# Performance work log

Measured on AMD Instinct MI355X. Metric: run time of the kernel, lower is better.

Reference implementation:

```python
import jax, jax.numpy as jnp
import numpy as np

B, D = 4096, 128
TAU_PLUS = 0.1
BETA = 1.0
TEMP = 0.5


def _normalize(x):
    return x / jnp.linalg.norm(x, axis=-1, keepdims=True)


def setup_inputs() -> dict:
    key = jax.random.key(0)
    k1, k2, k3, k4 = jax.random.split(key, 4)
    return {
        "img_z1": _normalize(jax.random.normal(k1, (B, D), dtype=jnp.float32)),
        "img_z2": _normalize(jax.random.normal(k2, (B, D), dtype=jnp.float32)),
        "text_z": _normalize(jax.random.normal(k3, (B, D), dtype=jnp.float32)),
        "attr_z": _normalize(jax.random.normal(k4, (B, D), dtype=jnp.float32)),
        "attr_uni": jnp.arange(B, dtype=jnp.int64),
    }


def _hard_negative_inter(o1, o2):
    # HardNegative_Inter with estimator='hard': only cross-modal negatives.
    b = o1.shape[0]
    n = b - 1
    sim = (o1 @ o2.T) / TEMP                       # [B, B]
    mask = ~jnp.eye(b, dtype=bool)                 # drop positive pair (i,i)
    neg = jnp.where(mask, jnp.exp(sim), 0.0)
    # imp = exp(beta * log(neg)) = exp(beta * sim) on masked entries
    imp = jnp.where(mask, jnp.exp(BETA * sim), 0.0)
    pos = jnp.exp(jnp.sum(o1 * o2, axis=-1) / TEMP)
    reweight_neg = jnp.sum(imp * neg, axis=-1) / (jnp.sum(imp, axis=-1) / n)
    ng = (-TAU_PLUS * n * pos + reweight_neg) / (1.0 - TAU_PLUS)
    ng = jnp.maximum(ng, n * np.e ** (-1.0 / TEMP))
    return jnp.mean(-jnp.log(pos / (pos + ng)))


def _hard_negative_intra(o1, o2):
    # HardNegative with estimator='hard': negatives over concat([o1, o2]).
    b = o1.shape[0]
    n = 2 * b - 2
    out = jnp.concatenate([o1, o2], axis=0)        # [2B, D]
    sim = (out @ out.T) / TEMP                     # [2B, 2B]
    idx = jnp.arange(2 * b)
    # mask zeros (i, i) and (i, i +/- B): entries with equal index mod B
    mask = (idx[:, None] % b) != (idx[None, :] % b)
    neg = jnp.where(mask, jnp.exp(sim), 0.0)
    imp = jnp.where(mask, jnp.exp(BETA * sim), 0.0)
    pos = jnp.exp(jnp.sum(o1 * o2, axis=-1) / TEMP)
    pos = jnp.concatenate([pos, pos], axis=0)      # [2B]
    reweight_neg = jnp.sum(imp * neg, axis=-1) / (jnp.sum(imp, axis=-1) / n)
    ng = (-TAU_PLUS * n * pos + reweight_neg) / (1.0 - TAU_PLUS)
    ng = jnp.maximum(ng, n * np.e ** (-1.0 / TEMP))
    return jnp.mean(-jnp.log(pos / (pos + ng)))


def reference(img_z1, img_z2, text_z, attr_z, attr_uni):
    # it/ta disabled (dummyzero); ia (inter) and ii (intra) enabled; numerator = 1
    a = attr_z[attr_uni, :]
    loss_i_a = 0.5 * (
        _hard_negative_inter(img_z1[attr_uni, :], a)
        + _hard_negative_inter(img_z2[attr_uni, :], a)
    )
    loss_inter_modal = loss_i_a / 1.0
    loss_intra_modal = _hard_negative_intra(img_z1, img_z2)
    return loss_inter_modal + loss_intra_modal
```

## Files before the change

### kernel.cpp

```cpp
#include <hip/hip_runtime.h>
#include <hip/hip_bf16.h>

#define BN 4096
#define DD 128

#define SQS 1.69864356f

typedef float f32x4 __attribute__((ext_vector_type(4)));
typedef int   i32x8 __attribute__((ext_vector_type(8)));
typedef int   i32x2 __attribute__((ext_vector_type(2)));

__device__ __forceinline__ float fast_exp2(float x) {
#if __has_builtin(__builtin_amdgcn_exp2f)
    return __builtin_amdgcn_exp2f(x);
#else
    float r;
    asm("v_exp_f32 %0, %1" : "=v"(r) : "v"(x));
    return r;
#endif
}

__global__ __launch_bounds__(256) void prep_kernel(
    const float* __restrict__ z1, const float* __restrict__ z2,
    const float* __restrict__ attr, const int* __restrict__ uni,
    char* __restrict__ Z1f, char* __restrict__ Z2f,
    char* __restrict__ G1f, char* __restrict__ G2f, char* __restrict__ Af,
    float* __restrict__ d1, float* __restrict__ d2, float* __restrict__ d3,
    float* __restrict__ S1, float* __restrict__ S2, float* __restrict__ out)
{
    int p = blockIdx.x;
    int t = threadIdx.x;
    int gid = p * 256 + t;
    if (gid < 4 * BN) { S1[gid] = 0.f; S2[gid] = 0.f; }
    if (gid == 0) out[0] = 0.f;

    int r = t >> 4, q = t & 15;
    int grow = p * 16 + r;
    int arow = uni[grow];

    __shared__ float lp[5][16][128];

    const float* sp[5] = { z1 + (size_t)grow * DD, z2 + (size_t)grow * DD,
                           z1 + (size_t)arow * DD, z2 + (size_t)arow * DD,
                           attr + (size_t)arow * DD };
    float v[5][8];
    #pragma unroll
    for (int m = 0; m < 5; m++) {
        const float4* s4 = (const float4*)(sp[m] + q * 8);
        #pragma unroll
        for (int i = 0; i < 2; i++) {
            float4 f = s4[i];
            v[m][4*i+0] = f.x; v[m][4*i+1] = f.y;
            v[m][4*i+2] = f.z; v[m][4*i+3] = f.w;
        }
    }
    float p1 = 0.f, p2 = 0.f, p3 = 0.f;
    #pragma unroll
    for (int e = 0; e < 8; e++) {
        p3 += v[0][e] * v[1][e];
        p1 += v[2][e] * v[4][e];
        p2 += v[3][e] * v[4][e];
    }
    #pragma unroll
    for (int m = 1; m < 16; m <<= 1) {
        p1 += __shfl_xor(p1, m);
        p2 += __shfl_xor(p2, m);
        p3 += __shfl_xor(p3, m);
    }
    if (q == 0) { d1[grow] = p1; d2[grow] = p2; d3[grow] = p3; }

    #pragma unroll
    for (int m = 0; m < 5; m++)
        #pragma unroll
        for (int e = 0; e < 8; e++)
            lp[m][r][q * 8 + e] = v[m][e] * SQS;
    __syncthreads();

    char* dsts[5] = { Z1f, Z2f, G1f, G2f, Af };
    int rw = (t >> 2) & 15;
    int k0 = 32 * (t >> 6) + (t & 3) * 8;
    #pragma unroll
    for (int m = 0; m < 5; m++) {
        const float* s = &lp[m][rw][k0];
        int w0 = __builtin_amdgcn_cvt_pk_fp8_f32(s[0], s[1], 0, false);
        w0     = __builtin_amdgcn_cvt_pk_fp8_f32(s[2], s[3], w0, true);
        int w1 = __builtin_amdgcn_cvt_pk_fp8_f32(s[4], s[5], 0, false);
        w1     = __builtin_amdgcn_cvt_pk_fp8_f32(s[6], s[7], w1, true);
        i32x2 w = { w0, w1 };
        *reinterpret_cast<i32x2*>(dsts[m] + (size_t)p * 2048 + (size_t)t * 8) = w;
    }
}

__global__ __launch_bounds__(256) void sweep_kernel(
    const char* __restrict__ Z1f, const char* __restrict__ Z2f,
    const char* __restrict__ G1f, const char* __restrict__ G2f,
    const char* __restrict__ Af,
    float* __restrict__ S1, float* __restrict__ S2)
{
    int gwid = blockIdx.x * 4 + (threadIdx.x >> 6);
    int lane = threadIdx.x & 63;

    int job, xblk, ychunk;
    const char *X, *Y;
    if (gwid < 1024) {
        job = gwid >> 9;
        int rem = gwid & 511;
        xblk = rem >> 3;
        ychunk = rem & 7;
        X = job ? G2f : G1f;
        Y = Af;
    } else {
        int g2 = gwid - 1024;
        job = 2 + (g2 >> 10);
        int rem = g2 & 1023;
        xblk = rem >> 4;
        int yc = rem & 15;
        X = (job == 2) ? Z1f : Z2f;
        Y = (yc < 8) ? Z1f : Z2f;
        ychunk = yc & 7;
    }

    size_t laneoff = (size_t)lane * 32;

    const char* xp = X + (size_t)(xblk * 4) * 2048 + laneoff;
    i32x8 xb0 = *reinterpret_cast<const i32x8*>(xp);
    i32x8 xb1 = *reinterpret_cast<const i32x8*>(xp + 2048);
    i32x8 xb2 = *reinterpret_cast<const i32x8*>(xp + 4096);
    i32x8 xb3 = *reinterpret_cast<const i32x8*>(xp + 6144);

    float a0e = 0.f, a0q = 0.f, a1e = 0.f, a1q = 0.f;
    float a2e = 0.f, a2q = 0.f, a3e = 0.f, a3q = 0.f;

    i32x8 yA, yB, yC;
    const char* yb0 = Y + (size_t)ychunk * 65536 + laneoff;

#define LOADY(BUF, PTR) BUF = *reinterpret_cast<const i32x8*>(PTR);

#define COMPY(BUF)                                                           \
    {                                                                        \
        f32x4 c0 = {0.f,0.f,0.f,0.f}, c1 = {0.f,0.f,0.f,0.f};                \
        f32x4 c2 = {0.f,0.f,0.f,0.f}, c3 = {0.f,0.f,0.f,0.f};                \
        c0 = __builtin_amdgcn_mfma_scale_f32_16x16x128_f8f6f4(               \
                 BUF, xb0, c0, 0, 0, 0, 0x7F7F7F7F, 0, 0x7F7F7F7F);          \
        c1 = __builtin_amdgcn_mfma_scale_f32_16x16x128_f8f6f4(               \
                 BUF, xb1, c1, 0, 0, 0, 0x7F7F7F7F, 0, 0x7F7F7F7F);          \
        c2 = __builtin_amdgcn_mfma_scale_f32_16x16x128_f8f6f4(               \
                 BUF, xb2, c2, 0, 0, 0, 0x7F7F7F7F, 0, 0x7F7F7F7F);          \
        c3 = __builtin_amdgcn_mfma_scale_f32_16x16x128_f8f6f4(               \
                 BUF, xb3, c3, 0, 0, 0, 0x7F7F7F7F, 0, 0x7F7F7F7F);          \
        _Pragma("unroll")                                                    \
        for (int q = 0; q < 4; q++) {                                        \
            float e0 = fast_exp2(c0[q]);                                     \
            a0e += e0; a0q = fmaf(e0, e0, a0q);                              \
            float e1 = fast_exp2(c1[q]);                                     \
            a1e += e1; a1q = fmaf(e1, e1, a1q);                              \
            float e2 = fast_exp2(c2[q]);                                     \
            a2e += e2; a2q = fmaf(e2, e2, a2q);                              \
            float e3 = fast_exp2(c3[q]);                                     \
            a3e += e3; a3q = fmaf(e3, e3, a3q);                              \
        }                                                                    \
    }

    LOADY(yA, yb0)
    LOADY(yB, yb0 + 2048)
    #pragma clang loop unroll(disable)
    for (int it = 0; it < 10; it++) {
        const char* pb = yb0 + (size_t)(3 * it) * 2048;
        LOADY(yC, pb + 2 * 2048)
        COMPY(yA)
        LOADY(yA, pb + 3 * 2048)
        COMPY(yB)
        LOADY(yB, pb + 4 * 2048)
        COMPY(yC)
    }
    COMPY(yA)
    COMPY(yB)
#undef LOADY
#undef COMPY

    #pragma unroll
    for (int k = 16; k <= 32; k <<= 1) {
        a0e += __shfl_xor(a0e, k); a0q += __shfl_xor(a0q, k);
        a1e += __shfl_xor(a1e, k); a1q += __shfl_xor(a1q, k);
        a2e += __shfl_xor(a2e, k); a2q += __shfl_xor(a2q, k);
        a3e += __shfl_xor(a3e, k); a3q += __shfl_xor(a3q, k);
    }
    if (lane < 16) {
        int base = job * BN + xblk * 64 + lane;
        atomicAdd(&S1[base],      a0e); atomicAdd(&S2[base],      a0q);
        atomicAdd(&S1[base + 16], a1e); atomicAdd(&S2[base + 16], a1q);
        atomicAdd(&S1[base + 32], a2e); atomicAdd(&S2[base + 32], a2q);
        atomicAdd(&S1[base + 48], a3e); atomicAdd(&S2[base + 48], a3q);
    }
}

__global__ __launch_bounds__(256) void finalize_kernel(
    const float* __restrict__ S1, const float* __restrict__ S2,
    const float* __restrict__ d1, const float* __restrict__ d2,
    const float* __restrict__ d3, float* __restrict__ out)
{
    int idx = blockIdx.x * 256 + threadIdx.x;
    float term = 0.f;
    const float EM2 = 0.13533528323661270f;
    if (idx < 8192) {
        int j = idx >> 12, i = idx & 4095;
        float dv = j ? d2[i] : d1[i];
        float n = 4095.f;
        float pos = __expf(2.f * dv);
        float s1 = S1[j * BN + i] - pos;
        float s2 = S2[j * BN + i] - pos * pos;
        float rw = s2 * n / s1;
        float ng = (-0.1f * n * pos + rw) * (1.f / 0.9f);
        ng = fmaxf(ng, n * EM2);
        term = logf((pos + ng) / pos) * (0.5f / 4096.f);
    } else {
        int i = idx - 8192;
        int ii = i & 4095;
        int job = 2 + (i >> 12);
        float n = 8190.f;
        const float E2 = 7.3890560989306495f, E4 = 54.598150033144236f;
        float pos = __expf(2.f * d3[ii]);
        float s1 = S1[job * BN + ii] - E2 - pos;
        float s2 = S2[job * BN + ii] - E4 - pos * pos;
        float rw = s2 * n / s1;
        float ng = (-0.1f * n * pos + rw) * (1.f / 0.9f);
        ng = fmaxf(ng, n * EM2);
        term = logf((pos + ng) / pos) * (1.f / 8192.f);
    }

    #pragma unroll
    for (int m = 1; m < 64; m <<= 1) term += __shfl_xor(term, m);
    __shared__ float sm[4];
    int wid = threadIdx.x >> 6;
    if ((threadIdx.x & 63) == 0) sm[wid] = term;
    __syncthreads();
    if (threadIdx.x == 0) atomicAdd(out, sm[0] + sm[1] + sm[2] + sm[3]);
}

extern "C" void kernel_launch(void* const* d_in, const int* in_sizes, int n_in,
                              void* d_out, int out_size, void* d_ws, size_t ws_size,
                              hipStream_t stream)
{
    const float* z1   = (const float*)d_in[0];
    const float* z2   = (const float*)d_in[1];
    const float* attr = (const float*)d_in[3];
    const int*   uni  = (const int*)d_in[4];
    float* out = (float*)d_out;

    char* ws = (char*)d_ws;
    size_t matb = (size_t)BN * DD;
    char* Z1f = ws;
    char* Z2f = Z1f + matb;
    char* G1f = Z2f + matb;
    char* G2f = G1f + matb;
    char* Af  = G2f + matb;
    float* S1 = (float*)(ws + 5 * matb);
    float* S2 = S1 + 4 * BN;
    float* d1 = S2 + 4 * BN;
    float* d2 = d1 + BN;
    float* d3 = d2 + BN;

    prep_kernel<<<256, 256, 0, stream>>>(z1, z2, attr, uni,
                                         Z1f, Z2f, G1f, G2f, Af,
                                         d1, d2, d3, S1, S2, out);
    sweep_kernel<<<768, 256, 0, stream>>>(Z1f, Z2f, G1f, G2f, Af, S1, S2);
    finalize_kernel<<<64, 256, 0, stream>>>(S1, S2, d1, d2, d3, out);
}
```

Baseline: 31.30 us.

## Halve per-wave Y chunk, double sweep grid, and pack exp accumulators as float2

Splits each wave's Y range in half (16 tiles instead of 32), doubling the sweep grid to 1536 blocks, so the kernel has more waves to spread across the CUs and better latency hiding. The per-lane accumulators become two-wide float vectors so the adds and FMAs can map to packed FP32 instructions. The cost is twice as many atomicAdds into S1/S2 and per-wave X-tile reloads, plus a shorter loop with less steady-state pipelining.

```diff
diff --git a/kernel.cpp b/kernel.cpp
--- a/kernel.cpp
+++ b/kernel.cpp
@@ -7,6 +7,7 @@
 #define SQS 1.69864356f
 
 typedef float f32x4 __attribute__((ext_vector_type(4)));
+typedef float f32x2 __attribute__((ext_vector_type(2)));
 typedef int   i32x8 __attribute__((ext_vector_type(8)));
 typedef int   i32x2 __attribute__((ext_vector_type(2)));
 
@@ -102,22 +103,22 @@
 
     int job, xblk, ychunk;
     const char *X, *Y;
-    if (gwid < 1024) {
-        job = gwid >> 9;
-        int rem = gwid & 511;
-        xblk = rem >> 3;
-        ychunk = rem & 7;
+    if (gwid < 2048) {
+        job = gwid >> 10;
+        int rem = gwid & 1023;
+        xblk = rem >> 4;
+        ychunk = rem & 15;
         X = job ? G2f : G1f;
         Y = Af;
     } else {
-        int g2 = gwid - 1024;
-        job = 2 + (g2 >> 10);
-        int rem = g2 & 1023;
-        xblk = rem >> 4;
-        int yc = rem & 15;
+        int g2 = gwid - 2048;
+        job = 2 + (g2 >> 11);
+        int rem = g2 & 2047;
+        xblk = rem >> 5;
+        int yc = rem & 31;
         X = (job == 2) ? Z1f : Z2f;
-        Y = (yc < 8) ? Z1f : Z2f;
-        ychunk = yc & 7;
+        Y = (yc < 16) ? Z1f : Z2f;
+        ychunk = yc & 15;
     }
 
     size_t laneoff = (size_t)lane * 32;
@@ -128,11 +129,11 @@
     i32x8 xb2 = *reinterpret_cast<const i32x8*>(xp + 4096);
     i32x8 xb3 = *reinterpret_cast<const i32x8*>(xp + 6144);
 
-    float a0e = 0.f, a0q = 0.f, a1e = 0.f, a1q = 0.f;
-    float a2e = 0.f, a2q = 0.f, a3e = 0.f, a3q = 0.f;
+    f32x2 a0e = {0.f,0.f}, a0q = {0.f,0.f}, a1e = {0.f,0.f}, a1q = {0.f,0.f};
+    f32x2 a2e = {0.f,0.f}, a2q = {0.f,0.f}, a3e = {0.f,0.f}, a3q = {0.f,0.f};
 
     i32x8 yA, yB, yC;
-    const char* yb0 = Y + (size_t)ychunk * 65536 + laneoff;
+    const char* yb0 = Y + (size_t)ychunk * 32768 + laneoff;
 
 #define LOADY(BUF, PTR) BUF = *reinterpret_cast<const i32x8*>(PTR);
 
@@ -149,22 +150,26 @@
         c3 = __builtin_amdgcn_mfma_scale_f32_16x16x128_f8f6f4(               \
                  BUF, xb3, c3, 0, 0, 0, 0x7F7F7F7F, 0, 0x7F7F7F7F);          \
         _Pragma("unroll")                                                    \
-        for (int q = 0; q < 4; q++) {                                        \
-            float e0 = fast_exp2(c0[q]);                                     \
-            a0e += e0; a0q = fmaf(e0, e0, a0q);                              \
-            float e1 = fast_exp2(c1[q]);                                     \
-            a1e += e1; a1q = fmaf(e1, e1, a1q);                              \
-            float e2 = fast_exp2(c2[q]);                                     \
-            a2e += e2; a2q = fmaf(e2, e2, a2q);                              \
-            float e3 = fast_exp2(c3[q]);                                     \
-            a3e += e3; a3q = fmaf(e3, e3, a3q);                              \
+        for (int q = 0; q < 2; q++) {                                        \
+            f32x2 e0 = { fast_exp2(c0[2*q]), fast_exp2(c0[2*q+1]) };         \
+            a0e += e0;                                                       \
+            a0q = __builtin_elementwise_fma(e0, e0, a0q);                    \
+            f32x2 e1 = { fast_exp2(c1[2*q]), fast_exp2(c1[2*q+1]) };         \
+            a1e += e1;                                                       \
+            a1q = __builtin_elementwise_fma(e1, e1, a1q);                    \
+            f32x2 e2 = { fast_exp2(c2[2*q]), fast_exp2(c2[2*q+1]) };         \
+            a2e += e2;                                                       \
+            a2q = __builtin_elementwise_fma(e2, e2, a2q);                    \
+            f32x2 e3 = { fast_exp2(c3[2*q]), fast_exp2(c3[2*q+1]) };         \
+            a3e += e3;                                                       \
+            a3q = __builtin_elementwise_fma(e3, e3, a3q);                    \
         }                                                                    \
     }
 
     LOADY(yA, yb0)
     LOADY(yB, yb0 + 2048)
     #pragma clang loop unroll(disable)
-    for (int it = 0; it < 10; it++) {
+    for (int it = 0; it < 4; it++) {
         const char* pb = yb0 + (size_t)(3 * it) * 2048;
         LOADY(yC, pb + 2 * 2048)
         COMPY(yA)
@@ -173,24 +178,32 @@
         LOADY(yB, pb + 4 * 2048)
         COMPY(yC)
     }
+    LOADY(yC, yb0 + 14 * 2048)
     COMPY(yA)
+    LOADY(yA, yb0 + 15 * 2048)
     COMPY(yB)
+    COMPY(yC)
+    COMPY(yA)
 #undef LOADY
 #undef COMPY
 
+    float r0e = a0e.x + a0e.y, r0q = a0q.x + a0q.y;
+    float r1e = a1e.x + a1e.y, r1q = a1q.x + a1q.y;
+    float r2e = a2e.x + a2e.y, r2q = a2q.x + a2q.y;
+    float r3e = a3e.x + a3e.y, r3q = a3q.x + a3q.y;
     #pragma unroll
     for (int k = 16; k <= 32; k <<= 1) {
-        a0e += __shfl_xor(a0e, k); a0q += __shfl_xor(a0q, k);
-        a1e += __shfl_xor(a1e, k); a1q += __shfl_xor(a1q, k);
-        a2e += __shfl_xor(a2e, k); a2q += __shfl_xor(a2q, k);
-        a3e += __shfl_xor(a3e, k); a3q += __shfl_xor(a3q, k);
+        r0e += __shfl_xor(r0e, k); r0q += __shfl_xor(r0q, k);
+        r1e += __shfl_xor(r1e, k); r1q += __shfl_xor(r1q, k);
+        r2e += __shfl_xor(r2e, k); r2q += __shfl_xor(r2q, k);
+        r3e += __shfl_xor(r3e, k); r3q += __shfl_xor(r3q, k);
     }
     if (lane < 16) {
         int base = job * BN + xblk * 64 + lane;
-        atomicAdd(&S1[base],      a0e); atomicAdd(&S2[base],      a0q);
-        atomicAdd(&S1[base + 16], a1e); atomicAdd(&S2[base + 16], a1q);
-        atomicAdd(&S1[base + 32], a2e); atomicAdd(&S2[base + 32], a2q);
-        atomicAdd(&S1[base + 48], a3e); atomicAdd(&S2[base + 48], a3q);
+        atomicAdd(&S1[base],      r0e); atomicAdd(&S2[base],      r0q);
+        atomicAdd(&S1[base + 16], r1e); atomicAdd(&S2[base + 16], r1q);
+        atomicAdd(&S1[base + 32], r2e); atomicAdd(&S2[base + 32], r2q);
+        atomicAdd(&S1[base + 48], r3e); atomicAdd(&S2[base + 48], r3q);
     }
 }
 
@@ -263,6 +276,6 @@
     prep_kernel<<<256, 256, 0, stream>>>(z1, z2, attr, uni,
                                          Z1f, Z2f, G1f, G2f, Af,
                                          d1, d2, d3, S1, S2, out);
-    sweep_kernel<<<768, 256, 0, stream>>>(Z1f, Z2f, G1f, G2f, Af, S1, S2);
+    sweep_kernel<<<1536, 256, 0, stream>>>(Z1f, Z2f, G1f, G2f, Af, S1, S2);
     finalize_kernel<<<64, 256, 0, stream>>>(S1, S2, d1, d2, d3, out);
 }
```

New measurement: 31.43 us. Within noise of the previous version (+0.4%).
